# Kernel tuning notes

Measured on AMD Instinct MI355X. Metric: run time of the kernel, lower is better.

Reference implementation:

```python
import jax, jax.numpy as jnp
import numpy as np

B, L, M, N, C = 2, 1024, 8, 16, 16
H, W, D = 64, 64, 16  # d == c: one histogram plane per feature channel


def setup_inputs() -> dict:
    key = jax.random.key(0)
    k1, k2, k3, k4, k5 = jax.random.split(key, 5)
    feats_src_dst = jax.random.normal(k1, (B, L, N, C), dtype=jnp.float32)
    voxels_src = jax.random.randint(k2, (B, L, 2), 0, 64).astype(jnp.int32)
    voxels_dst = jax.random.randint(k3, (B, L, 2), 0, 64).astype(jnp.int32)
    idxs_src = jax.random.randint(k4, (B, L, M), 0, L).astype(jnp.int32)
    idxs_dst = jax.random.randint(k5, (B, L, N), 0, L).astype(jnp.int32)
    return {
        "feats_src_dst": feats_src_dst,
        "voxels_src": voxels_src,
        "voxels_dst": voxels_dst,
        "idxs_src": idxs_src,
        "idxs_dst": idxs_dst,
    }


def reference(feats_src_dst, voxels_src, voxels_dst, idxs_src, idxs_dst):
    b, l, m = idxs_src.shape
    n = idxs_dst.shape[-1]
    c = feats_src_dst.shape[-1]
    dt = feats_src_dst.dtype

    gather = jax.vmap(lambda arr, idx: arr[idx])  # per-batch fancy gather

    s = idxs_src                                   # [b,l,m]  src KNN of each anchor
    dd = gather(idxs_dst, s)                       # [b,l,m,n] dst KNN of each src neighbor
    vsrc = gather(voxels_src.astype(dt), s)        # [b,l,m,2]
    vdst = gather(voxels_dst.astype(dt), dd)       # [b,l,m,n,2]
    wf = gather(feats_src_dst, s)                  # [b,l,m,n,c] vote weights

    # translation -> centered histogram bin
    t = vdst - vsrc[:, :, :, None, :]              # [b,l,m,n,2] (y,x)
    by = jnp.floor(t[..., 0]).astype(jnp.int32) + H // 2
    bx = jnp.floor(t[..., 1]).astype(jnp.int32) + W // 2
    valid = (by >= 0) & (by < H) & (bx >= 0) & (bx < W)
    by = jnp.clip(by, 0, H - 1)
    bx = jnp.clip(bx, 0, W - 1)
    wf = jnp.where(valid[..., None], wf, jnp.zeros((), dt))

    bi = jnp.broadcast_to(jnp.arange(b)[:, None, None, None], (b, l, m, n))
    li = jnp.broadcast_to(jnp.arange(l)[None, :, None, None], (b, l, m, n))

    hist = jnp.zeros((b, l, H, W, c), dt)
    hist = hist.at[bi, li, by, bx].add(wf)         # scatter-add voting
    return jnp.transpose(hist, (0, 1, 4, 2, 3))    # [b,l,c,h,w]
```

## Files before the change

kernel.cpp:

```cpp
#include <hip/hip_runtime.h>

#define B_ 2
#define L_ 1024
#define M_ 8
#define N_ 16
#define C_ 16
#define H_ 64
#define W_ 64

#define NVOTE (M_ * N_)
#define PLANE (H_ * W_)

__global__ __launch_bounds__(256) void hough_vote_plane_kernel(
    const float* __restrict__ feats,
    const int*   __restrict__ voxels_src,
    const int*   __restrict__ voxels_dst,
    const int*   __restrict__ idxs_src,
    const int*   __restrict__ idxs_dst,
    float*       __restrict__ out)
{
    const int gb  = blockIdx.x;
    const int bl  = gb >> 4;
    const int c   = gb & (C_ - 1);
    const int b   = bl >> 10;
    const int tid = threadIdx.x;

    __shared__ float s_plane[PLANE];

    float w   = 0.f;
    int   bin = -1;
    if (tid < NVOTE) {
        int m    = tid >> 4;
        int n    = tid & (N_ - 1);
        int s    = idxs_src[bl * M_ + m];
        int base = b * L_ + s;
        int2 vs  = ((const int2*)voxels_src)[base];
        int  dd  = idxs_dst[base * N_ + n];
        int2 vd  = ((const int2*)voxels_dst)[b * L_ + dd];
        int by = vd.x - vs.x + H_ / 2;
        int bx = vd.y - vs.y + W_ / 2;
        if (by >= 0 && by < H_ && bx >= 0 && bx < W_) {
            bin = by * W_ + bx;
            w   = feats[((size_t)base * N_ + n) * C_ + c];
        }
    }

    float4* p4 = (float4*)s_plane;
    #pragma unroll
    for (int i = 0; i < PLANE / 4 / 256; ++i)
        p4[i * 256 + tid] = make_float4(0.f, 0.f, 0.f, 0.f);
    __syncthreads();

    if (bin >= 0) atomicAdd(&s_plane[bin], w);
    __syncthreads();

    float4* o4 = (float4*)(out + ((size_t)bl * C_ + c) * PLANE);
    #pragma unroll
    for (int i = 0; i < PLANE / 4 / 256; ++i)
        o4[i * 256 + tid] = p4[i * 256 + tid];
}

extern "C" void kernel_launch(void* const* d_in, const int* in_sizes, int n_in,
                              void* d_out, int out_size, void* d_ws, size_t ws_size,
                              hipStream_t stream) {
    const float* feats      = (const float*)d_in[0];
    const int*   voxels_src = (const int*)d_in[1];
    const int*   voxels_dst = (const int*)d_in[2];
    const int*   idxs_src   = (const int*)d_in[3];
    const int*   idxs_dst   = (const int*)d_in[4];
    float*       out        = (float*)d_out;

    hough_vote_plane_kernel<<<B_ * L_ * C_, 256, 0, stream>>>(
        feats, voxels_src, voxels_dst, idxs_src, idxs_dst, out);
}
```

Measured before the change: 528.2 us.

## Process all channels per anchor in one block with reused index gather

Each block now handles one (batch, anchor) pair and loops over all 16 channels. Gather indices and bins are computed once, and a full 16-float feature vector is loaded per vote. The single shared plane is zeroed again and reused for each channel. A custom barrier waits only on LDS/scalar counters, not on global stores, so output writes can overlap later channels. Launch bounds request higher occupancy. The cost is 16 serialized barrier phases per block and a 16x smaller grid.

```diff
diff --git a/kernel.cpp b/kernel.cpp
--- a/kernel.cpp
+++ b/kernel.cpp
@@ -11,7 +11,16 @@
 #define NVOTE (M_ * N_)
 #define PLANE (H_ * W_)
 
-__global__ __launch_bounds__(256) void hough_vote_plane_kernel(
+typedef float vf4  __attribute__((ext_vector_type(4)));
+typedef float vf16 __attribute__((ext_vector_type(16)));
+
+__device__ __forceinline__ void bar_nodrain() {
+    asm volatile("s_waitcnt lgkmcnt(0)" ::: "memory");
+    __builtin_amdgcn_s_barrier();
+    asm volatile("" ::: "memory");
+}
+
+__global__ __launch_bounds__(256, 8) void hough_vote_bl_kernel(
     const float* __restrict__ feats,
     const int*   __restrict__ voxels_src,
     const int*   __restrict__ voxels_dst,
@@ -19,45 +28,53 @@
     const int*   __restrict__ idxs_dst,
     float*       __restrict__ out)
 {
-    const int gb  = blockIdx.x;
-    const int bl  = gb >> 4;
-    const int c   = gb & (C_ - 1);
+    const int bl  = blockIdx.x;
     const int b   = bl >> 10;
     const int tid = threadIdx.x;
 
     __shared__ float s_plane[PLANE];
+    vf4* p4 = (vf4*)s_plane;
 
-    float w   = 0.f;
-    int   bin = -1;
+    int  bin = -1;
+    vf16 wv;
     if (tid < NVOTE) {
-        int m    = tid >> 4;
-        int n    = tid & (N_ - 1);
-        int s    = idxs_src[bl * M_ + m];
-        int base = b * L_ + s;
-        int2 vs  = ((const int2*)voxels_src)[base];
-        int  dd  = idxs_dst[base * N_ + n];
-        int2 vd  = ((const int2*)voxels_dst)[b * L_ + dd];
-        int by = vd.x - vs.x + H_ / 2;
-        int bx = vd.y - vs.y + W_ / 2;
-        if (by >= 0 && by < H_ && bx >= 0 && bx < W_) {
+        const int m    = tid >> 4;
+        const int n    = tid & (N_ - 1);
+        const int s    = idxs_src[bl * M_ + m];
+        const int base = b * L_ + s;
+        const int2 vs  = ((const int2*)voxels_src)[base];
+        const int  dd  = idxs_dst[base * N_ + n];
+        const int2 vd  = ((const int2*)voxels_dst)[b * L_ + dd];
+        wv = *(const vf16*)(feats + ((size_t)base * N_ + n) * C_);
+        const int by = vd.x - vs.x + H_ / 2;
+        const int bx = vd.y - vs.y + W_ / 2;
+        if (by >= 0 && by < H_ && bx >= 0 && bx < W_)
             bin = by * W_ + bx;
-            w   = feats[((size_t)base * N_ + n) * C_ + c];
-        }
     }
 
-    float4* p4 = (float4*)s_plane;
+    const vf4 z = {0.f, 0.f, 0.f, 0.f};
     #pragma unroll
     for (int i = 0; i < PLANE / 4 / 256; ++i)
-        p4[i * 256 + tid] = make_float4(0.f, 0.f, 0.f, 0.f);
-    __syncthreads();
+        p4[i * 256 + tid] = z;
+    bar_nodrain();
 
-    if (bin >= 0) atomicAdd(&s_plane[bin], w);
-    __syncthreads();
+    vf4* o4base = (vf4*)(out + (size_t)bl * C_ * PLANE);
 
-    float4* o4 = (float4*)(out + ((size_t)bl * C_ + c) * PLANE);
     #pragma unroll
-    for (int i = 0; i < PLANE / 4 / 256; ++i)
-        o4[i * 256 + tid] = p4[i * 256 + tid];
+    for (int c = 0; c < C_; ++c) {
+        if (bin >= 0) atomicAdd(&s_plane[bin], wv[c]);
+        bar_nodrain();
+
+        vf4* o4 = o4base + c * (PLANE / 4);
+        #pragma unroll
+        for (int i = 0; i < PLANE / 4 / 256; ++i) {
+            const int idx = i * 256 + tid;
+            vf4 v = p4[idx];
+            o4[idx] = v;
+            if (c < C_ - 1) p4[idx] = z;
+        }
+        bar_nodrain();
+    }
 }
 
 extern "C" void kernel_launch(void* const* d_in, const int* in_sizes, int n_in,
@@ -70,6 +87,6 @@
     const int*   idxs_dst   = (const int*)d_in[4];
     float*       out        = (float*)d_out;
 
-    hough_vote_plane_kernel<<<B_ * L_ * C_, 256, 0, stream>>>(
+    hough_vote_bl_kernel<<<B_ * L_, 256, 0, stream>>>(
         feats, voxels_src, voxels_dst, idxs_src, idxs_dst, out);
 }
```

Result: no change. 529.6 us (+0.3%).
